# Kernel tuning notes

Hardware: AMD Instinct MI355X
Metric: run time of the kernel (lower is better)

## Reference

```python
import jax, jax.numpy as jnp
import numpy as np

EPS_BN = 1e-5

def conv1(W, x):
    # 1x1 conv1d, no bias: W (Cout,Cin), x (B,Cin,N)
    return jnp.einsum('oc,bcn->bon', W, x)

def bn(x, g, b):
    # training-mode BatchNorm1d over (batch, points) per channel
    m = jnp.mean(x, axis=(0, 2), keepdims=True)
    v = jnp.mean((x - m) ** 2, axis=(0, 2), keepdims=True)
    return g[None, :, None] * (x - m) / jnp.sqrt(v + EPS_BN) + b[None, :, None]

def three_interpolation(p_dense, p_sparse, f_sparse):
    # p_dense (B,N1,3), p_sparse (B,N2,3), f_sparse (B,C,N2) -> (B,C,N1)
    d2 = jnp.sum((p_dense[:, :, None, :] - p_sparse[:, None, :, :]) ** 2, axis=-1)  # (B,N1,N2)
    neg, idx = jax.lax.top_k(-d2, 3)  # 3 nearest neighbors, (B,N1,3)
    w = 1.0 / (jnp.maximum(-neg, 0.0) + 1e-8)  # inverse (squared) distance, as pointnet2 three_nn
    w = w / jnp.sum(w, axis=-1, keepdims=True)
    gathered = jax.vmap(lambda f, i: f[:, i])(f_sparse, idx)  # (B,C,N1,3)
    return jnp.einsum('bcnk,bnk->bcn', gathered, w)

def fp(p_dense, f_skip, p_sparse, f_sparse, W1, g1, b1, W2, g2, b2):
    # FeaturePropogation upsample branch: concat(skip, interp) -> [conv1d+BN] x decoder_layers (act_args=None)
    x = jnp.concatenate([f_skip, three_interpolation(p_dense, p_sparse, f_sparse)], axis=1)
    x = bn(conv1(W1, x), g1, b1)
    x = bn(conv1(W2, x), g2, b2)
    return x

def setup_inputs():
    key = jax.random.key(0)
    ks = iter(jax.random.split(key, 40))
    B, N = 4, 8192
    Ns = [N, N, 2048, 512, 128]      # point counts of p0..p4 (strides 4)
    Cs = [128, 256, 512, 1024]       # encoder_channel_list
    d = {}
    for i in range(5):
        d[f'p{i}'] = jax.random.normal(next(ks), (B, Ns[i], 3), jnp.float32)
    for i in range(4):
        d[f'f{i + 1}'] = jax.random.normal(next(ks), (B, Cs[i], Ns[i + 1]), jnp.float32)
    d['cls_label'] = jax.random.randint(next(ks), (B, 1), 0, 16)
    # class-label convs: 16 -> 64 (BN+GELU) -> C0
    d['Wc1'] = jax.random.normal(next(ks), (64, 16), jnp.float32) * 0.1
    d['gc'] = jax.random.uniform(next(ks), (64,), jnp.float32, 0.5, 1.5)
    d['bc'] = jax.random.normal(next(ks), (64,), jnp.float32) * 0.1
    d['Wc2'] = jax.random.normal(next(ks), (Cs[0], 64), jnp.float32) * 0.1
    # decoder stages, coarsest (s2) to finest (s0)
    ins = [Cs[2] + Cs[3], Cs[1] + Cs[2], Cs[0] + Cs[1]]
    outs = [Cs[2], Cs[1], Cs[0]]
    for tag, ci, co in zip(['s2', 's1', 's0'], ins, outs):
        d[f'W{tag}a'] = jax.random.normal(next(ks), (co, ci), jnp.float32) * 0.05
        d[f'g{tag}a'] = jax.random.uniform(next(ks), (co,), jnp.float32, 0.5, 1.5)
        d[f'b{tag}a'] = jax.random.normal(next(ks), (co,), jnp.float32) * 0.1
        d[f'W{tag}b'] = jax.random.normal(next(ks), (co, co), jnp.float32) * 0.05
        d[f'g{tag}b'] = jax.random.uniform(next(ks), (co,), jnp.float32, 0.5, 1.5)
        d[f'b{tag}b'] = jax.random.normal(next(ks), (co,), jnp.float32) * 0.1
    return d

def reference(p0, p1, p2, p3, p4, f1, f2, f3, f4, cls_label,
              Wc1, gc, bc, Wc2,
              Ws2a, gs2a, bs2a, Ws2b, gs2b, bs2b,
              Ws1a, gs1a, bs1a, Ws1b, gs1b, bs1b,
              Ws0a, gs0a, bs0a, Ws0b, gs0b, bs0b):
    B, N = p0.shape[0], p0.shape[1]
    # one-hot class embedding broadcast over points, mapped 16 -> 64 -> C0
    one_hot = jax.nn.one_hot(cls_label[:, 0], 16, dtype=f1.dtype)  # (B,16)
    cls_feat = jnp.broadcast_to(one_hot[:, :, None], (B, 16, N))
    cls_feat = conv1(Wc2, jax.nn.gelu(bn(conv1(Wc1, cls_feat), gc, bc), approximate=False))
    # decoder stages, coarse to fine
    f3n = fp(p3, f3, p4, f4, Ws2a, gs2a, bs2a, Ws2b, gs2b, bs2b)   # (B,512,512)
    f2n = fp(p2, f2, p3, f3n, Ws1a, gs1a, bs1a, Ws1b, gs1b, bs1b)  # (B,256,2048)
    f1n = fp(p1, f1 + cls_feat, p2, f2n, Ws0a, gs0a, bs0a, Ws0b, gs0b, bs0b)  # (B,128,8192)
    return f1n
```

## Files before the change

### kernel.cpp

```cpp
#include <hip/hip_runtime.h>
#include <math.h>

#define BN_EPS 1e-5f

typedef float f32x4 __attribute__((ext_vector_type(4)));
typedef short s16x8 __attribute__((ext_vector_type(8)));

__device__ __forceinline__ unsigned short f2bf(float f) {
    unsigned u = __builtin_bit_cast(unsigned, f);
    u = u + 0x7FFFu + ((u >> 16) & 1u);
    return (unsigned short)(u >> 16);
}
__device__ __forceinline__ float bf2f(unsigned short s) {
    unsigned u = ((unsigned)s) << 16;
    return __builtin_bit_cast(float, u);
}

__device__ __forceinline__ void gload16(const void* g, void* l) {
    __builtin_amdgcn_global_load_lds((const __attribute__((address_space(1))) unsigned int*)g,
                                     (__attribute__((address_space(3))) unsigned int*)l,
                                     16, 0, 0);
}

template<int CAND, int CHUNK, int STRIDE, bool PART>
__device__ __forceinline__ void knn_body(const float* __restrict__ pd,
                                         const float* __restrict__ ps,
                                         int N1, int N2total, int grp, int slice, int b,
                                         int* __restrict__ idx, float* __restrict__ w,
                                         unsigned long long* __restrict__ pk, int nslice,
                                         float* spx, float* spy, float* spz) {
    int tid = threadIdx.x;
    int cbase = slice * CAND;
    for (int g = tid; g < CAND; g += 256) {
        int s = g / CHUNK, off = g % CHUNK;
        size_t base = ((size_t)b * N2total + cbase + g) * 3;
        spx[s * STRIDE + off] = ps[base];
        spy[s * STRIDE + off] = ps[base + 1];
        spz[s * STRIDE + off] = ps[base + 2];
    }
    __syncthreads();
    int sub = tid & 7;
    int n = grp * 32 + (tid >> 3);
    size_t pb = ((size_t)b * N1 + n) * 3;
    float px = pd[pb], py = pd[pb + 1], pz = pd[pb + 2];
    float dd0 = 3.4e38f, dd1 = 3.4e38f, dd2 = 3.4e38f;
    int ii0 = 0, ii1 = 0, ii2 = 0;
    const float* rx = spx + sub * STRIDE;
    const float* ry = spy + sub * STRIDE;
    const float* rz = spz + sub * STRIDE;
    int jbase = cbase + sub * CHUNK;
    for (int t = 0; t < CHUNK; t += 4) {
        f32x4 x4 = *(const f32x4*)(rx + t);
        f32x4 y4 = *(const f32x4*)(ry + t);
        f32x4 z4 = *(const f32x4*)(rz + t);
#pragma unroll
        for (int e = 0; e < 4; e++) {
            float dx = px - x4[e], dy = py - y4[e], dz = pz - z4[e];
            float d = dx * dx + dy * dy + dz * dz;
            int j = jbase + t + e;
            bool C0 = d < dd0, C1 = d < dd1, C2 = d < dd2;
            int ni2 = C1 ? ii1 : (C2 ? j : ii2);
            int ni1 = C0 ? ii0 : (C1 ? j : ii1);
            int ni0 = C0 ? j : ii0;
            dd2 = __builtin_amdgcn_fmed3f(d, dd1, dd2);
            dd1 = __builtin_amdgcn_fmed3f(d, dd0, dd1);
            dd0 = fminf(d, dd0);
            ii0 = ni0; ii1 = ni1; ii2 = ni2;
        }
    }
    unsigned long long k0 = ((unsigned long long)__builtin_bit_cast(unsigned, dd0) << 32) | (unsigned)ii0;
    unsigned long long k1 = ((unsigned long long)__builtin_bit_cast(unsigned, dd1) << 32) | (unsigned)ii1;
    unsigned long long k2 = ((unsigned long long)__builtin_bit_cast(unsigned, dd2) << 32) | (unsigned)ii2;
#pragma unroll
    for (int m = 1; m < 8; m <<= 1) {
        unsigned long long e0, e1, e2;
        { int lo = __shfl_xor((int)(unsigned)(k0 & 0xFFFFFFFFull), m), hi = __shfl_xor((int)(unsigned)(k0 >> 32), m);
          e0 = ((unsigned long long)(unsigned)hi << 32) | (unsigned)lo; }
        { int lo = __shfl_xor((int)(unsigned)(k1 & 0xFFFFFFFFull), m), hi = __shfl_xor((int)(unsigned)(k1 >> 32), m);
          e1 = ((unsigned long long)(unsigned)hi << 32) | (unsigned)lo; }
        { int lo = __shfl_xor((int)(unsigned)(k2 & 0xFFFFFFFFull), m), hi = __shfl_xor((int)(unsigned)(k2 >> 32), m);
          e2 = ((unsigned long long)(unsigned)hi << 32) | (unsigned)lo; }
        unsigned long long t0, t1;
        t0 = k0 > e0 ? k0 : e0; k0 = k0 < e0 ? k0 : e0; t1 = k1 > t0 ? k1 : t0; k1 = k1 < t0 ? k1 : t0; k2 = k2 < t1 ? k2 : t1;
        t0 = k0 > e1 ? k0 : e1; k0 = k0 < e1 ? k0 : e1; t1 = k1 > t0 ? k1 : t0; k1 = k1 < t0 ? k1 : t0; k2 = k2 < t1 ? k2 : t1;
        t0 = k0 > e2 ? k0 : e2; k0 = k0 < e2 ? k0 : e2; t1 = k1 > t0 ? k1 : t0; k1 = k1 < t0 ? k1 : t0; k2 = k2 < t1 ? k2 : t1;
    }
    if (sub == 0) {
        if (PART) {
            size_t o = ((size_t)(b * N1 + n) * nslice + slice) * 3;
            pk[o] = k0; pk[o + 1] = k1; pk[o + 2] = k2;
        } else {
            float f0 = __builtin_bit_cast(float, (unsigned)(k0 >> 32));
            float f1 = __builtin_bit_cast(float, (unsigned)(k1 >> 32));
            float f2 = __builtin_bit_cast(float, (unsigned)(k2 >> 32));
            float w0 = 1.f / (f0 + 1e-8f), w1 = 1.f / (f1 + 1e-8f), w2 = 1.f / (f2 + 1e-8f);
            float s = 1.f / (w0 + w1 + w2);
            size_t o = ((size_t)b * N1 + n) * 3;
            idx[o] = (int)(unsigned)(k0 & 0xFFFFFFFFull);
            idx[o + 1] = (int)(unsigned)(k1 & 0xFFFFFFFFull);
            idx[o + 2] = (int)(unsigned)(k2 & 0xFFFFFFFFull);
            w[o] = w0 * s; w[o + 1] = w1 * s; w[o + 2] = w2 * s;
        }
    }
}

__global__ __launch_bounds__(256) void prep(const float* __restrict__ f1,
                                            const float* __restrict__ f2,
                                            const float* __restrict__ f3,
                                            const float* __restrict__ f4,
                                            unsigned short* __restrict__ F1T,
                                            unsigned short* __restrict__ F2T,
                                            unsigned short* __restrict__ F3T,
                                            unsigned short* __restrict__ F4T,
                                            const int* __restrict__ lbl,
                                            const float* __restrict__ Wc1,
                                            const float* __restrict__ gc,
                                            const float* __restrict__ bc,
                                            const float* __restrict__ Wc2,
                                            const float* __restrict__ p1,
                                            const float* __restrict__ p2,
                                            const float* __restrict__ p3,
                                            const float* __restrict__ p4,
                                            int* __restrict__ idx1, float* __restrict__ w1,
                                            int* __restrict__ idx2, float* __restrict__ w2,
                                            unsigned long long* __restrict__ pk0,
                                            const float* __restrict__ Ws2a,
                                            unsigned short* __restrict__ WI2, float* __restrict__ BIA2,
                                            unsigned short* __restrict__ WS2, float* __restrict__ BIS2,
                                            const float* __restrict__ Ws1a,
                                            unsigned short* __restrict__ WS1, float* __restrict__ BIS1,
                                            const float* __restrict__ Ws0a,
                                            unsigned short* __restrict__ WS0, float* __restrict__ BIS0) {
    __shared__ float t[32][33];
    __shared__ float clsv[32];
    __shared__ float hsh[4][64];
    __shared__ float actsh[4][64];
    __shared__ float spx[8 * 72], spy[8 * 72], spz[8 * 72];
    int bx = blockIdx.x, b = blockIdx.y;
    int tid = threadIdx.x;

    if (bx >= 3024) {
        if (b != 0) return;
        int wx = bx - 3024;
        const float* W; unsigned short* Wb; float* bias; int Ktot, kOff, Ks, m;
        if (wx < 512)       { W = Ws2a; Wb = WI2; bias = BIA2; Ktot = 1536; kOff = 512; Ks = 1024; m = wx; }
        else if (wx < 1024) { W = Ws2a; Wb = WS2; bias = BIS2; Ktot = 1536; kOff = 0;   Ks = 512;  m = wx - 512; }
        else if (wx < 1280) { W = Ws1a; Wb = WS1; bias = BIS1; Ktot = 768;  kOff = 0;   Ks = 256;  m = wx - 1024; }
        else                { W = Ws0a; Wb = WS0; bias = BIS0; Ktot = 384;  kOff = 0;   Ks = 128;  m = wx - 1280; }
        for (int k = tid; k < Ks; k += 256)
            Wb[(size_t)m * Ks + k] = f2bf(W[(size_t)m * Ktot + kOff + k]);
        if (tid == 0) bias[m] = 0.f;
        return;
    }
    if (bx >= 1920) {
        int kx = bx - 1920;
        if (kx < 16)      knn_body<128, 16, 24, false>(p3, p4, 512, 128, kx, 0, b, idx2, w2, nullptr, 1, spx, spy, spz);
        else if (kx < 80) knn_body<512, 64, 72, false>(p2, p3, 2048, 512, kx - 16, 0, b, idx1, w1, nullptr, 1, spx, spy, spz);
        else {
            int u = kx - 80;
            knn_body<512, 64, 72, true>(p1, p2, 8192, 2048, u >> 2, u & 3, b, nullptr, nullptr, pk0, 4, spx, spy, spz);
        }
        return;
    }
    const float* in; unsigned short* out; int C, N, nx, seg; bool docls = false;
    if (bx < 128)      { in = f4; out = F4T; C = 1024; N = 128;  nx = 4;   seg = bx; }
    else if (bx < 384) { in = f3; out = F3T; C = 512;  N = 512;  nx = 16;  seg = bx - 128; }
    else if (bx < 896) { in = f2; out = F2T; C = 256;  N = 2048; nx = 64;  seg = bx - 384; }
    else               { in = f1; out = F1T; C = 128;  N = 8192; nx = 256; seg = bx - 896; docls = true; }
    int n0 = (seg % nx) * 32, c0 = (seg / nx) * 32;
    if (docls) {
        { int b2 = tid >> 6, c = tid & 63; hsh[b2][c] = Wc1[c * 16 + lbl[b2]]; }
        __syncthreads();
        if (tid < 64) {
            int c = tid;
            float m = 0.f;
            for (int b2 = 0; b2 < 4; b2++) m += hsh[b2][c];
            m *= 0.25f;
            float v = 0.f;
            for (int b2 = 0; b2 < 4; b2++) { float d = hsh[b2][c] - m; v += d * d; }
            v *= 0.25f;
            float sc = gc[c] * rsqrtf(v + BN_EPS);
            float sh = bc[c] - m * sc;
            for (int b2 = 0; b2 < 4; b2++) {
                float x = hsh[b2][c] * sc + sh;
                actsh[b2][c] = 0.5f * x * (1.f + erff(x * 0.70710678118654752f));
            }
        }
        __syncthreads();
        if (tid < 32) {
            float s = 0.f;
            for (int c = 0; c < 64; c++) s += Wc2[(size_t)(c0 + tid) * 64 + c] * actsh[b][c];
            clsv[tid] = s;
        }
        __syncthreads();
    }
    int i = tid & 31, jj = tid >> 5;
#pragma unroll
    for (int j = jj; j < 32; j += 8) {
        float v = in[((size_t)b * C + c0 + j) * N + n0 + i];
        if (docls) v += clsv[j];
        t[j][i] = v;
    }
    __syncthreads();
    int j2 = tid & 31, i2b = tid >> 5;
#pragma unroll
    for (int i2 = i2b; i2 < 32; i2 += 8)
        out[((size_t)b * N + n0 + i2) * C + c0 + j2] = f2bf(t[j2][i2]);
}

__global__ __launch_bounds__(256) void knn_merge(const unsigned long long* __restrict__ pk,
                                                 int* __restrict__ idx, float* __restrict__ w,
                                                 int NQ) {
    int q = blockIdx.x * 256 + threadIdx.x;
    if (q >= NQ) return;
    const unsigned long long* p = pk + (size_t)q * 12;
    unsigned long long k0 = ~0ull, k1 = ~0ull, k2 = ~0ull;
#pragma unroll
    for (int i = 0; i < 12; i++) {
        unsigned long long c = p[i];
        unsigned long long t0 = k0 > c ? k0 : c; k0 = k0 < c ? k0 : c;
        unsigned long long t1 = k1 > t0 ? k1 : t0; k1 = k1 < t0 ? k1 : t0;
        k2 = k2 < t1 ? k2 : t1;
    }
    float f0 = __builtin_bit_cast(float, (unsigned)(k0 >> 32));
    float f1 = __builtin_bit_cast(float, (unsigned)(k1 >> 32));
    float f2 = __builtin_bit_cast(float, (unsigned)(k2 >> 32));
    float w0 = 1.f / (f0 + 1e-8f), w1 = 1.f / (f1 + 1e-8f), w2 = 1.f / (f2 + 1e-8f);
    float s = 1.f / (w0 + w1 + w2);
    size_t o = (size_t)q * 3;
    idx[o] = (int)(unsigned)(k0 & 0xFFFFFFFFull);
    idx[o + 1] = (int)(unsigned)(k1 & 0xFFFFFFFFull);
    idx[o + 2] = (int)(unsigned)(k2 & 0xFFFFFFFFull);
    w[o] = w0 * s; w[o + 1] = w1 * s; w[o + 2] = w2 * s;
}

__global__ __launch_bounds__(256) void wprep(const float* __restrict__ W,
                                             const float* __restrict__ sc,
                                             const float* __restrict__ sh,
                                             unsigned short* __restrict__ Wb,
                                             float* __restrict__ bias,
                                             int Ktot, int kOff, int Ks) {
    int m = blockIdx.x;
    int tid = threadIdx.x;
    float bsum = 0.f;
    for (int k = tid; k < Ks; k += 256) {
        float wv = W[(size_t)m * Ktot + kOff + k];
        Wb[(size_t)m * Ks + k] = f2bf(wv * sc[k]);
        bsum += wv * sh[k];
    }
    __shared__ float ls[256];
    ls[tid] = bsum;
    __syncthreads();
    for (int o = 128; o > 0; o >>= 1) {
        if (tid < o) ls[tid] += ls[tid + o];
        __syncthreads();
    }
    if (tid == 0) bias[m] = ls[0];
}

template<bool GATHER, bool WRSTATS>
__global__ __launch_bounds__(256) void gemm64(const unsigned short* __restrict__ XT,
                                              const unsigned short* __restrict__ Wb,
                                              const float* __restrict__ bias,
                                              const unsigned short* __restrict__ G,
                                              const int* __restrict__ gidx,
                                              const float* __restrict__ gw,
                                              int n1shift, int N2loc,
                                              unsigned short* __restrict__ OutT,
                                              float* __restrict__ ps,
                                              int BN, int K, int M) {
    __shared__ unsigned short As[2][64 * 32];
    __shared__ unsigned short Bs[2][64 * 32];
    __shared__ float sred[2][2][32][2];
    int tid = threadIdx.x;
    int lane = tid & 63, wid = tid >> 6;
    int wn = wid & 1, wm = wid >> 1;
    int bx = blockIdx.x, by = blockIdx.y;

    int srow = (wid << 4) + (lane >> 2);
    int skcol = (lane & 3) << 3;
    const unsigned short* gA = XT + (size_t)(bx * 64 + srow) * K + skcol;
    const unsigned short* gB = Wb + (size_t)(by * 64 + srow) * K + skcol;

    int r16 = lane & 15, q = lane >> 4;
    f32x4 acc[2][2];
#pragma unroll
    for (int i = 0; i < 2; i++)
#pragma unroll
        for (int j = 0; j < 2; j++) acc[i][j] = (f32x4)0.f;

    int nt = K >> 5;
    gload16(gA, &As[0][wid * 512]);
    gload16(gB, &Bs[0][wid * 512]);

    for (int t = 0; t < nt; t++) {
        int cur = t & 1;
        if (t + 1 < nt) {
            int k0 = (t + 1) << 5;
            gload16(gA + k0, &As[cur ^ 1][wid * 512]);
            gload16(gB + k0, &Bs[cur ^ 1][wid * 512]);
            asm volatile("s_waitcnt vmcnt(2)" ::: "memory");
        } else {
            asm volatile("s_waitcnt vmcnt(0)" ::: "memory");
        }
        __syncthreads();
        s16x8 afr[2], bfr[2];
        afr[0] = *(const s16x8*)&As[cur][(wn * 32 + r16) * 32 + q * 8];
        afr[1] = *(const s16x8*)&As[cur][(wn * 32 + 16 + r16) * 32 + q * 8];
        bfr[0] = *(const s16x8*)&Bs[cur][(wm * 32 + r16) * 32 + q * 8];
        bfr[1] = *(const s16x8*)&Bs[cur][(wm * 32 + 16 + r16) * 32 + q * 8];
        asm volatile("s_waitcnt lgkmcnt(0)" ::: "memory");
        __builtin_amdgcn_sched_barrier(0);
        __syncthreads();
#pragma unroll
        for (int i = 0; i < 2; i++)
#pragma unroll
            for (int j = 0; j < 2; j++)
                acc[i][j] = __builtin_amdgcn_mfma_f32_16x16x32_bf16(afr[i], bfr[j], acc[i][j], 0, 0, 0);
    }

    if (GATHER) {
#pragma unroll
        for (int i = 0; i < 2; i++)
#pragma unroll
            for (int rr = 0; rr < 4; rr++) {
                int R = bx * 64 + wn * 32 + i * 16 + q * 4 + rr;
                size_t ob = (size_t)R * 3;
                int i0 = gidx[ob], i1 = gidx[ob + 1], i2 = gidx[ob + 2];
                float w0 = gw[ob], w1 = gw[ob + 1], w2 = gw[ob + 2];
                size_t gbase = (size_t)(R >> n1shift) * N2loc;
                const unsigned short* g0 = G + (gbase + i0) * M + by * 64;
                const unsigned short* g1 = G + (gbase + i1) * M + by * 64;
                const unsigned short* g2 = G + (gbase + i2) * M + by * 64;
#pragma unroll
                for (int j = 0; j < 2; j++) {
                    int mcol = wm * 32 + j * 16 + r16;
                    acc[i][j][rr] += w0 * bf2f(g0[mcol]) + w1 * bf2f(g1[mcol]) + w2 * bf2f(g2[mcol]);
                }
            }
    }

    int mc0 = by * 64 + wm * 32 + r16;
    float bv[2] = { bias[mc0], bias[mc0 + 16] };
    unsigned short* Ob = OutT + (size_t)(bx * 64) * M + by * 64;
    float s[2] = {0.f, 0.f}, qq[2] = {0.f, 0.f};
#pragma unroll
    for (int i = 0; i < 2; i++) {
#pragma unroll
        for (int j = 0; j < 2; j++) {
            int mcol = wm * 32 + j * 16 + r16;
#pragma unroll
            for (int r = 0; r < 4; r++) {
                float v = acc[i][j][r] + bv[j];
                s[j] += v; qq[j] += v * v;
                int n = wn * 32 + i * 16 + q * 4 + r;
                Ob[(size_t)n * M + mcol] = f2bf(v);
            }
        }
    }
    if (WRSTATS) {
#pragma unroll
        for (int j = 0; j < 2; j++) {
            s[j] += __shfl_xor(s[j], 16); s[j] += __shfl_xor(s[j], 32);
            qq[j] += __shfl_xor(qq[j], 16); qq[j] += __shfl_xor(qq[j], 32);
        }
        if (lane < 16) {
#pragma unroll
            for (int j = 0; j < 2; j++) {
                sred[wn][wm][j * 16 + lane][0] = s[j];
                sred[wn][wm][j * 16 + lane][1] = qq[j];
            }
        }
        __syncthreads();
        if (tid < 64) {
            int wmm = tid >> 5, c = tid & 31;
            float ssum = sred[0][wmm][c][0] + sred[1][wmm][c][0];
            float qsum = sred[0][wmm][c][1] + sred[1][wmm][c][1];
            size_t blin = (size_t)by * gridDim.x + bx;
            ps[blin * 128 + tid * 2] = ssum;
            ps[blin * 128 + tid * 2 + 1] = qsum;
        }
    }
}

__global__ __launch_bounds__(256) void bn_finalize(const float* __restrict__ ps,
                                                   const float* __restrict__ g,
                                                   const float* __restrict__ bb,
                                                   float* __restrict__ sc,
                                                   float* __restrict__ sh,
                                                   int gx, int Npts) {
    int m = blockIdx.x;
    int by = m >> 6, ch = m & 63;
    float s = 0.f, q = 0.f;
    for (int bxi = threadIdx.x; bxi < gx; bxi += 256) {
        size_t blin = (size_t)by * gx + bxi;
        s += ps[blin * 128 + ch * 2];
        q += ps[blin * 128 + ch * 2 + 1];
    }
    __shared__ float ls[256], lq[256];
    ls[threadIdx.x] = s; lq[threadIdx.x] = q;
    __syncthreads();
    for (int o = 128; o > 0; o >>= 1) {
        if (threadIdx.x < o) { ls[threadIdx.x] += ls[threadIdx.x + o]; lq[threadIdx.x] += lq[threadIdx.x + o]; }
        __syncthreads();
    }
    if (threadIdx.x == 0) {
        float inv = 1.f / (float)Npts;
        float mean = ls[0] * inv;
        float var = fmaxf(lq[0] * inv - mean * mean, 0.f);
        float scale = g[m] * rsqrtf(var + BN_EPS);
        sc[m] = scale;
        sh[m] = bb[m] - mean * scale;
    }
}

__global__ __launch_bounds__(256) void out_bn_tr(const unsigned short* __restrict__ in,
                                                 float* __restrict__ out,
                                                 const float* __restrict__ sc,
                                                 const float* __restrict__ sh,
                                                 int M, int N) {
    __shared__ float t[32][33];
    int b = blockIdx.z;
    int n0 = blockIdx.x * 32, m0 = blockIdx.y * 32;
    int j = threadIdx.x & 31, ii = threadIdx.x >> 5;
#pragma unroll
    for (int i = ii; i < 32; i += 8)
        t[i][j] = bf2f(in[((size_t)b * N + n0 + i) * M + m0 + j]);
    __syncthreads();
    int i2 = threadIdx.x & 31, j2b = threadIdx.x >> 5;
#pragma unroll
    for (int j2 = j2b; j2 < 32; j2 += 8)
        out[((size_t)b * M + m0 + j2) * N + n0 + i2] = t[i2][j2] * sc[m0 + j2] + sh[m0 + j2];
}

extern "C" void kernel_launch(void* const* d_in, const int* in_sizes, int n_in,
                              void* d_out, int out_size, void* d_ws, size_t ws_size,
                              hipStream_t stream) {
    const float* p1 = (const float*)d_in[1];
    const float* p2 = (const float*)d_in[2];
    const float* p3 = (const float*)d_in[3];
    const float* p4 = (const float*)d_in[4];
    const float* f1 = (const float*)d_in[5];
    const float* f2 = (const float*)d_in[6];
    const float* f3 = (const float*)d_in[7];
    const float* f4 = (const float*)d_in[8];
    const int* cls = (const int*)d_in[9];
    const float* Wc1 = (const float*)d_in[10];
    const float* gc  = (const float*)d_in[11];
    const float* bc  = (const float*)d_in[12];
    const float* Wc2 = (const float*)d_in[13];
    const float* Ws2a = (const float*)d_in[14];
    const float* gs2a = (const float*)d_in[15];
    const float* bs2a = (const float*)d_in[16];
    const float* Ws2b = (const float*)d_in[17];
    const float* gs2b = (const float*)d_in[18];
    const float* bs2b = (const float*)d_in[19];
    const float* Ws1a = (const float*)d_in[20];
    const float* gs1a = (const float*)d_in[21];
    const float* bs1a = (const float*)d_in[22];
    const float* Ws1b = (const float*)d_in[23];
    const float* gs1b = (const float*)d_in[24];
    const float* bs1b = (const float*)d_in[25];
    const float* Ws0a = (const float*)d_in[26];
    const float* gs0a = (const float*)d_in[27];
    const float* bs0a = (const float*)d_in[28];
    const float* Ws0b = (const float*)d_in[29];
    const float* gs0b = (const float*)d_in[30];
    const float* bs0b = (const float*)d_in[31];

    char* ws = (char*)d_ws;
    size_t off = 0;
    auto alloc = [&](size_t bytes) { char* p = ws + off; off += (bytes + 255) & ~(size_t)255; return p; };
    unsigned short* F4T = (unsigned short*)alloc((size_t)4 * 128 * 1024 * 2);
    unsigned short* F3T = (unsigned short*)alloc((size_t)4 * 512 * 512 * 2);
    unsigned short* F2T = (unsigned short*)alloc((size_t)4 * 2048 * 256 * 2);
    unsigned short* F1T = (unsigned short*)alloc((size_t)4 * 8192 * 128 * 2);
    unsigned short* G2T = (unsigned short*)alloc((size_t)4 * 128 * 512 * 2);
    unsigned short* G1T = (unsigned short*)alloc((size_t)4 * 512 * 256 * 2);
    unsigned short* G0T = (unsigned short*)alloc((size_t)4 * 2048 * 128 * 2);
    unsigned short* YA  = (unsigned short*)alloc((size_t)4 * 8192 * 128 * 2);
    unsigned short* FN2 = (unsigned short*)alloc((size_t)4 * 512 * 512 * 2);
    unsigned short* FN1 = (unsigned short*)alloc((size_t)4 * 2048 * 256 * 2);
    unsigned short* XO  = (unsigned short*)alloc((size_t)4 * 8192 * 128 * 2);
    unsigned short* WI2 = (unsigned short*)alloc((size_t)512 * 1024 * 2);
    unsigned short* WS2 = (unsigned short*)alloc((size_t)512 * 512 * 2);
    unsigned short* WB2b = (unsigned short*)alloc((size_t)512 * 512 * 2);
    unsigned short* WI1 = (unsigned short*)alloc((size_t)256 * 512 * 2);
    unsigned short* WS1 = (unsigned short*)alloc((size_t)256 * 256 * 2);
    unsigned short* WB1b = (unsigned short*)alloc((size_t)256 * 256 * 2);
    unsigned short* WI0 = (unsigned short*)alloc((size_t)128 * 256 * 2);
    unsigned short* WS0 = (unsigned short*)alloc((size_t)128 * 128 * 2);
    unsigned short* WB0b = (unsigned short*)alloc((size_t)128 * 128 * 2);
    float* BIA2 = (float*)alloc(512 * 4); float* BIS2 = (float*)alloc(512 * 4);
    float* BI2b = (float*)alloc(512 * 4);
    float* BIA1 = (float*)alloc(256 * 4); float* BIS1 = (float*)alloc(256 * 4);
    float* BI1b = (float*)alloc(256 * 4);
    float* BIA0 = (float*)alloc(128 * 4); float* BIS0 = (float*)alloc(128 * 4);
    float* BI0b = (float*)alloc(128 * 4);
    int*   IDX0 = (int*)alloc((size_t)4 * 8192 * 3 * 4);
    float* WGT0 = (float*)alloc((size_t)4 * 8192 * 3 * 4);
    int*   IDX1 = (int*)alloc((size_t)4 * 2048 * 3 * 4);
    float* WGT1 = (float*)alloc((size_t)4 * 2048 * 3 * 4);
    int*   IDX2 = (int*)alloc((size_t)4 * 512 * 3 * 4);
    float* WGT2 = (float*)alloc((size_t)4 * 512 * 3 * 4);
    unsigned long long* PK0 = (unsigned long long*)alloc((size_t)4 * 8192 * 4 * 3 * 8);
    float* PS = (float*)alloc((size_t)1024 * 128 * 4);
    float* SC2a = (float*)alloc(512 * 4); float* SH2a = (float*)alloc(512 * 4);
    float* SC2b = (float*)alloc(512 * 4); float* SH2b = (float*)alloc(512 * 4);
    float* SC1a = (float*)alloc(512 * 4); float* SH1a = (float*)alloc(512 * 4);
    float* SC1b = (float*)alloc(512 * 4); float* SH1b = (float*)alloc(512 * 4);
    float* SC0a = (float*)alloc(512 * 4); float* SH0a = (float*)alloc(512 * 4);
    float* SC0b = (float*)alloc(512 * 4); float* SH0b = (float*)alloc(512 * 4);
    float* OUT = (float*)d_out;

    prep<<<dim3(4432, 4), 256, 0, stream>>>(f1, f2, f3, f4, F1T, F2T, F3T, F4T,
                                            cls, Wc1, gc, bc, Wc2,
                                            p1, p2, p3, p4,
                                            IDX1, WGT1, IDX2, WGT2, PK0,
                                            Ws2a, WI2, BIA2, WS2, BIS2,
                                            Ws1a, WS1, BIS1, Ws0a, WS0, BIS0);
    knn_merge<<<(4 * 8192) / 256, 256, 0, stream>>>(PK0, IDX0, WGT0, 4 * 8192);

    gemm64<false, false><<<dim3(8, 8), 256, 0, stream>>>(F4T, WI2, BIA2, nullptr, nullptr, nullptr, 0, 0,
                                                         G2T, nullptr, 512, 1024, 512);
    gemm64<true, true><<<dim3(32, 8), 256, 0, stream>>>(F3T, WS2, BIS2, G2T, IDX2, WGT2, 9, 128,
                                                        YA, PS, 2048, 512, 512);
    bn_finalize<<<512, 256, 0, stream>>>(PS, gs2a, bs2a, SC2a, SH2a, 32, 2048);
    wprep<<<512, 256, 0, stream>>>(Ws2b, SC2a, SH2a, WB2b, BI2b, 512, 0, 512);
    gemm64<false, true><<<dim3(32, 8), 256, 0, stream>>>(YA, WB2b, BI2b, nullptr, nullptr, nullptr, 0, 0,
                                                         FN2, PS, 2048, 512, 512);
    bn_finalize<<<512, 256, 0, stream>>>(PS, gs2b, bs2b, SC2b, SH2b, 32, 2048);

    wprep<<<256, 256, 0, stream>>>(Ws1a, SC2b, SH2b, WI1, BIA1, 768, 256, 512);
    gemm64<false, false><<<dim3(32, 4), 256, 0, stream>>>(FN2, WI1, BIA1, nullptr, nullptr, nullptr, 0, 0,
                                                          G1T, nullptr, 2048, 512, 256);
    gemm64<true, true><<<dim3(128, 4), 256, 0, stream>>>(F2T, WS1, BIS1, G1T, IDX1, WGT1, 11, 512,
                                                         YA, PS, 8192, 256, 256);
    bn_finalize<<<256, 256, 0, stream>>>(PS, gs1a, bs1a, SC1a, SH1a, 128, 8192);
    wprep<<<256, 256, 0, stream>>>(Ws1b, SC1a, SH1a, WB1b, BI1b, 256, 0, 256);
    gemm64<false, true><<<dim3(128, 4), 256, 0, stream>>>(YA, WB1b, BI1b, nullptr, nullptr, nullptr, 0, 0,
                                                          FN1, PS, 8192, 256, 256);
    bn_finalize<<<256, 256, 0, stream>>>(PS, gs1b, bs1b, SC1b, SH1b, 128, 8192);

    wprep<<<128, 256, 0, stream>>>(Ws0a, SC1b, SH1b, WI0, BIA0, 384, 128, 256);
    gemm64<false, false><<<dim3(128, 2), 256, 0, stream>>>(FN1, WI0, BIA0, nullptr, nullptr, nullptr, 0, 0,
                                                           G0T, nullptr, 8192, 256, 128);
    gemm64<true, true><<<dim3(512, 2), 256, 0, stream>>>(F1T, WS0, BIS0, G0T, IDX0, WGT0, 13, 2048,
                                                         YA, PS, 32768, 128, 128);
    bn_finalize<<<128, 256, 0, stream>>>(PS, gs0a, bs0a, SC0a, SH0a, 512, 32768);
    wprep<<<128, 256, 0, stream>>>(Ws0b, SC0a, SH0a, WB0b, BI0b, 128, 0, 128);
    gemm64<false, true><<<dim3(512, 2), 256, 0, stream>>>(YA, WB0b, BI0b, nullptr, nullptr, nullptr, 0, 0,
                                                          XO, PS, 32768, 128, 128);
    bn_finalize<<<128, 256, 0, stream>>>(PS, gs0b, bs0b, SC0b, SH0b, 512, 32768);

    out_bn_tr<<<dim3(8192 / 32, 128 / 32, 4), 256, 0, stream>>>(XO, OUT, SC0b, SH0b, 128, 8192);
}
```

Before: 186.8 us.

## Fuse BN finalize into weight prep and drop the separate kNN merge kernel

The finest-level kNN no longer splits candidates into four slices with a separate merge kernel. Each block now loops over all 2048 sparse points in LDS-staged slices, writing indices and weights directly. Separately, the bn_finalize kernels that fed the weight folding are merged into a new wprep_fin kernel, which reduces the partial sums itself before scaling the weights. This cuts about ten launches and an intermediate buffer, but every wprep_fin block recomputes the BN statistics redundantly, and the kNN now runs with four times fewer blocks, each doing four times the work.

```diff
diff --git a/kernel.cpp b/kernel.cpp
--- a/kernel.cpp
+++ b/kernel.cpp
@@ -22,50 +22,51 @@
                                      16, 0, 0);
 }
 
-template<int CAND, int CHUNK, int STRIDE, bool PART>
-__device__ __forceinline__ void knn_body(const float* __restrict__ pd,
+template<int N2TOT, int SLICE, int CHUNK, int STRIDE>
+__device__ __forceinline__ void knn_full(const float* __restrict__ pd,
                                          const float* __restrict__ ps,
-                                         int N1, int N2total, int grp, int slice, int b,
+                                         int N1, int grp, int b,
                                          int* __restrict__ idx, float* __restrict__ w,
-                                         unsigned long long* __restrict__ pk, int nslice,
                                          float* spx, float* spy, float* spz) {
     int tid = threadIdx.x;
-    int cbase = slice * CAND;
-    for (int g = tid; g < CAND; g += 256) {
-        int s = g / CHUNK, off = g % CHUNK;
-        size_t base = ((size_t)b * N2total + cbase + g) * 3;
-        spx[s * STRIDE + off] = ps[base];
-        spy[s * STRIDE + off] = ps[base + 1];
-        spz[s * STRIDE + off] = ps[base + 2];
-    }
-    __syncthreads();
     int sub = tid & 7;
     int n = grp * 32 + (tid >> 3);
     size_t pb = ((size_t)b * N1 + n) * 3;
     float px = pd[pb], py = pd[pb + 1], pz = pd[pb + 2];
     float dd0 = 3.4e38f, dd1 = 3.4e38f, dd2 = 3.4e38f;
     int ii0 = 0, ii1 = 0, ii2 = 0;
-    const float* rx = spx + sub * STRIDE;
-    const float* ry = spy + sub * STRIDE;
-    const float* rz = spz + sub * STRIDE;
-    int jbase = cbase + sub * CHUNK;
-    for (int t = 0; t < CHUNK; t += 4) {
-        f32x4 x4 = *(const f32x4*)(rx + t);
-        f32x4 y4 = *(const f32x4*)(ry + t);
-        f32x4 z4 = *(const f32x4*)(rz + t);
-#pragma unroll
-        for (int e = 0; e < 4; e++) {
-            float dx = px - x4[e], dy = py - y4[e], dz = pz - z4[e];
-            float d = dx * dx + dy * dy + dz * dz;
-            int j = jbase + t + e;
-            bool C0 = d < dd0, C1 = d < dd1, C2 = d < dd2;
-            int ni2 = C1 ? ii1 : (C2 ? j : ii2);
-            int ni1 = C0 ? ii0 : (C1 ? j : ii1);
-            int ni0 = C0 ? j : ii0;
-            dd2 = __builtin_amdgcn_fmed3f(d, dd1, dd2);
-            dd1 = __builtin_amdgcn_fmed3f(d, dd0, dd1);
-            dd0 = fminf(d, dd0);
-            ii0 = ni0; ii1 = ni1; ii2 = ni2;
+    for (int sb = 0; sb < N2TOT; sb += SLICE) {
+        __syncthreads();
+        for (int g = tid; g < SLICE; g += 256) {
+            int s = g / CHUNK, off = g % CHUNK;
+            size_t base = ((size_t)b * N2TOT + sb + g) * 3;
+            spx[s * STRIDE + off] = ps[base];
+            spy[s * STRIDE + off] = ps[base + 1];
+            spz[s * STRIDE + off] = ps[base + 2];
+        }
+        __syncthreads();
+        const float* rx = spx + sub * STRIDE;
+        const float* ry = spy + sub * STRIDE;
+        const float* rz = spz + sub * STRIDE;
+        int jbase = sb + sub * CHUNK;
+        for (int t = 0; t < CHUNK; t += 4) {
+            f32x4 x4 = *(const f32x4*)(rx + t);
+            f32x4 y4 = *(const f32x4*)(ry + t);
+            f32x4 z4 = *(const f32x4*)(rz + t);
+#pragma unroll
+            for (int e = 0; e < 4; e++) {
+                float dx = px - x4[e], dy = py - y4[e], dz = pz - z4[e];
+                float d = dx * dx + dy * dy + dz * dz;
+                int j = jbase + t + e;
+                bool C0 = d < dd0, C1 = d < dd1, C2 = d < dd2;
+                int ni2 = C1 ? ii1 : (C2 ? j : ii2);
+                int ni1 = C0 ? ii0 : (C1 ? j : ii1);
+                int ni0 = C0 ? j : ii0;
+                dd2 = __builtin_amdgcn_fmed3f(d, dd1, dd2);
+                dd1 = __builtin_amdgcn_fmed3f(d, dd0, dd1);
+                dd0 = fminf(d, dd0);
+                ii0 = ni0; ii1 = ni1; ii2 = ni2;
+            }
         }
     }
     unsigned long long k0 = ((unsigned long long)__builtin_bit_cast(unsigned, dd0) << 32) | (unsigned)ii0;
@@ -86,21 +87,16 @@
         t0 = k0 > e2 ? k0 : e2; k0 = k0 < e2 ? k0 : e2; t1 = k1 > t0 ? k1 : t0; k1 = k1 < t0 ? k1 : t0; k2 = k2 < t1 ? k2 : t1;
     }
     if (sub == 0) {
-        if (PART) {
-            size_t o = ((size_t)(b * N1 + n) * nslice + slice) * 3;
-            pk[o] = k0; pk[o + 1] = k1; pk[o + 2] = k2;
-        } else {
-            float f0 = __builtin_bit_cast(float, (unsigned)(k0 >> 32));
-            float f1 = __builtin_bit_cast(float, (unsigned)(k1 >> 32));
-            float f2 = __builtin_bit_cast(float, (unsigned)(k2 >> 32));
-            float w0 = 1.f / (f0 + 1e-8f), w1 = 1.f / (f1 + 1e-8f), w2 = 1.f / (f2 + 1e-8f);
-            float s = 1.f / (w0 + w1 + w2);
-            size_t o = ((size_t)b * N1 + n) * 3;
-            idx[o] = (int)(unsigned)(k0 & 0xFFFFFFFFull);
-            idx[o + 1] = (int)(unsigned)(k1 & 0xFFFFFFFFull);
-            idx[o + 2] = (int)(unsigned)(k2 & 0xFFFFFFFFull);
-            w[o] = w0 * s; w[o + 1] = w1 * s; w[o + 2] = w2 * s;
-        }
+        float f0 = __builtin_bit_cast(float, (unsigned)(k0 >> 32));
+        float f1 = __builtin_bit_cast(float, (unsigned)(k1 >> 32));
+        float f2 = __builtin_bit_cast(float, (unsigned)(k2 >> 32));
+        float w0 = 1.f / (f0 + 1e-8f), w1 = 1.f / (f1 + 1e-8f), w2 = 1.f / (f2 + 1e-8f);
+        float s = 1.f / (w0 + w1 + w2);
+        size_t o = ((size_t)b * N1 + n) * 3;
+        idx[o] = (int)(unsigned)(k0 & 0xFFFFFFFFull);
+        idx[o + 1] = (int)(unsigned)(k1 & 0xFFFFFFFFull);
+        idx[o + 2] = (int)(unsigned)(k2 & 0xFFFFFFFFull);
+        w[o] = w0 * s; w[o + 1] = w1 * s; w[o + 2] = w2 * s;
     }
 }
 
@@ -121,9 +117,9 @@
                                             const float* __restrict__ p2,
                                             const float* __restrict__ p3,
                                             const float* __restrict__ p4,
+                                            int* __restrict__ idx0, float* __restrict__ w0,
                                             int* __restrict__ idx1, float* __restrict__ w1,
                                             int* __restrict__ idx2, float* __restrict__ w2,
-                                            unsigned long long* __restrict__ pk0,
                                             const float* __restrict__ Ws2a,
                                             unsigned short* __restrict__ WI2, float* __restrict__ BIA2,
                                             unsigned short* __restrict__ WS2, float* __restrict__ BIS2,
@@ -139,9 +135,9 @@
     int bx = blockIdx.x, b = blockIdx.y;
     int tid = threadIdx.x;
 
-    if (bx >= 3024) {
+    if (bx >= 2256) {
         if (b != 0) return;
-        int wx = bx - 3024;
+        int wx = bx - 2256;
         const float* W; unsigned short* Wb; float* bias; int Ktot, kOff, Ks, m;
         if (wx < 512)       { W = Ws2a; Wb = WI2; bias = BIA2; Ktot = 1536; kOff = 512; Ks = 1024; m = wx; }
         else if (wx < 1024) { W = Ws2a; Wb = WS2; bias = BIS2; Ktot = 1536; kOff = 0;   Ks = 512;  m = wx - 512; }
@@ -154,12 +150,9 @@
     }
     if (bx >= 1920) {
         int kx = bx - 1920;
-        if (kx < 16)      knn_body<128, 16, 24, false>(p3, p4, 512, 128, kx, 0, b, idx2, w2, nullptr, 1, spx, spy, spz);
-        else if (kx < 80) knn_body<512, 64, 72, false>(p2, p3, 2048, 512, kx - 16, 0, b, idx1, w1, nullptr, 1, spx, spy, spz);
-        else {
-            int u = kx - 80;
-            knn_body<512, 64, 72, true>(p1, p2, 8192, 2048, u >> 2, u & 3, b, nullptr, nullptr, pk0, 4, spx, spy, spz);
-        }
+        if (kx < 16)      knn_full<128, 128, 16, 24>(p3, p4, 512, kx, b, idx2, w2, spx, spy, spz);
+        else if (kx < 80) knn_full<512, 512, 64, 72>(p2, p3, 2048, kx - 16, b, idx1, w1, spx, spy, spz);
+        else              knn_full<2048, 512, 64, 72>(p1, p2, 8192, kx - 80, b, idx0, w0, spx, spy, spz);
         return;
     }
     const float* in; unsigned short* out; int C, N, nx, seg; bool docls = false;
@@ -208,45 +201,41 @@
         out[((size_t)b * N + n0 + i2) * C + c0 + j2] = f2bf(t[j2][i2]);
 }
 
-__global__ __launch_bounds__(256) void knn_merge(const unsigned long long* __restrict__ pk,
-                                                 int* __restrict__ idx, float* __restrict__ w,
-                                                 int NQ) {
-    int q = blockIdx.x * 256 + threadIdx.x;
-    if (q >= NQ) return;
-    const unsigned long long* p = pk + (size_t)q * 12;
-    unsigned long long k0 = ~0ull, k1 = ~0ull, k2 = ~0ull;
-#pragma unroll
-    for (int i = 0; i < 12; i++) {
-        unsigned long long c = p[i];
-        unsigned long long t0 = k0 > c ? k0 : c; k0 = k0 < c ? k0 : c;
-        unsigned long long t1 = k1 > t0 ? k1 : t0; k1 = k1 < t0 ? k1 : t0;
-        k2 = k2 < t1 ? k2 : t1;
-    }
-    float f0 = __builtin_bit_cast(float, (unsigned)(k0 >> 32));
-    float f1 = __builtin_bit_cast(float, (unsigned)(k1 >> 32));
-    float f2 = __builtin_bit_cast(float, (unsigned)(k2 >> 32));
-    float w0 = 1.f / (f0 + 1e-8f), w1 = 1.f / (f1 + 1e-8f), w2 = 1.f / (f2 + 1e-8f);
-    float s = 1.f / (w0 + w1 + w2);
-    size_t o = (size_t)q * 3;
-    idx[o] = (int)(unsigned)(k0 & 0xFFFFFFFFull);
-    idx[o + 1] = (int)(unsigned)(k1 & 0xFFFFFFFFull);
-    idx[o + 2] = (int)(unsigned)(k2 & 0xFFFFFFFFull);
-    w[o] = w0 * s; w[o + 1] = w1 * s; w[o + 2] = w2 * s;
-}
-
-__global__ __launch_bounds__(256) void wprep(const float* __restrict__ W,
-                                             const float* __restrict__ sc,
-                                             const float* __restrict__ sh,
-                                             unsigned short* __restrict__ Wb,
-                                             float* __restrict__ bias,
-                                             int Ktot, int kOff, int Ks) {
-    int m = blockIdx.x;
-    int tid = threadIdx.x;
+__global__ __launch_bounds__(256) void wprep_fin(const float* __restrict__ W,
+                                                 const float* __restrict__ ps,
+                                                 const float* __restrict__ g,
+                                                 const float* __restrict__ bb,
+                                                 unsigned short* __restrict__ Wb,
+                                                 float* __restrict__ bias,
+                                                 int Ktot, int kOff, int Ks,
+                                                 int gx, int Npts) {
+    __shared__ float scl[1024], shl[1024];
+    int m = blockIdx.x, tid = threadIdx.x;
+    for (int k0 = 0; k0 < Ks; k0 += 256) {
+        int k = k0 + tid;
+        if (k < Ks) {
+            float s = 0.f, q = 0.f;
+            size_t rowbase = (size_t)(k >> 6) * gx;
+            int ch2 = (k & 63) * 2;
+            for (int bxi = 0; bxi < gx; bxi++) {
+                size_t blin = rowbase + bxi;
+                s += ps[blin * 128 + ch2];
+                q += ps[blin * 128 + ch2 + 1];
+            }
+            float inv = 1.f / (float)Npts;
+            float mean = s * inv;
+            float var = fmaxf(q * inv - mean * mean, 0.f);
+            float scale = g[k] * rsqrtf(var + BN_EPS);
+            scl[k] = scale;
+            shl[k] = bb[k] - mean * scale;
+        }
+    }
+    __syncthreads();
     float bsum = 0.f;
     for (int k = tid; k < Ks; k += 256) {
         float wv = W[(size_t)m * Ktot + kOff + k];
-        Wb[(size_t)m * Ks + k] = f2bf(wv * sc[k]);
-        bsum += wv * sh[k];
+        Wb[(size_t)m * Ks + k] = f2bf(wv * scl[k]);
+        bsum += wv * shl[k];
     }
     __shared__ float ls[256];
     ls[tid] = bsum;
@@ -503,52 +492,40 @@
     float* WGT1 = (float*)alloc((size_t)4 * 2048 * 3 * 4);
     int*   IDX2 = (int*)alloc((size_t)4 * 512 * 3 * 4);
     float* WGT2 = (float*)alloc((size_t)4 * 512 * 3 * 4);
-    unsigned long long* PK0 = (unsigned long long*)alloc((size_t)4 * 8192 * 4 * 3 * 8);
     float* PS = (float*)alloc((size_t)1024 * 128 * 4);
-    float* SC2a = (float*)alloc(512 * 4); float* SH2a = (float*)alloc(512 * 4);
-    float* SC2b = (float*)alloc(512 * 4); float* SH2b = (float*)alloc(512 * 4);
-    float* SC1a = (float*)alloc(512 * 4); float* SH1a = (float*)alloc(512 * 4);
-    float* SC1b = (float*)alloc(512 * 4); float* SH1b = (float*)alloc(512 * 4);
-    float* SC0a = (float*)alloc(512 * 4); float* SH0a = (float*)alloc(512 * 4);
     float* SC0b = (float*)alloc(512 * 4); float* SH0b = (float*)alloc(512 * 4);
     float* OUT = (float*)d_out;
 
-    prep<<<dim3(4432, 4), 256, 0, stream>>>(f1, f2, f3, f4, F1T, F2T, F3T, F4T,
+    prep<<<dim3(3664, 4), 256, 0, stream>>>(f1, f2, f3, f4, F1T, F2T, F3T, F4T,
                                             cls, Wc1, gc, bc, Wc2,
                                             p1, p2, p3, p4,
-                                            IDX1, WGT1, IDX2, WGT2, PK0,
+                                            IDX0, WGT0, IDX1, WGT1, IDX2, WGT2,
                                             Ws2a, WI2, BIA2, WS2, BIS2,
                                             Ws1a, WS1, BIS1, Ws0a, WS0, BIS0);
-    knn_merge<<<(4 * 8192) / 256, 256, 0, stream>>>(PK0, IDX0, WGT0, 4 * 8192);
 
     gemm64<false, false><<<dim3(8, 8), 256, 0, stream>>>(F4T, WI2, BIA2, nullptr, nullptr, nullptr, 0, 0,
                                                          G2T, nullptr, 512, 1024, 512);
     gemm64<true, true><<<dim3(32, 8), 256, 0, stream>>>(F3T, WS2, BIS2, G2T, IDX2, WGT2, 9, 128,
                                                         YA, PS, 2048, 512, 512);
-    bn_finalize<<<512, 256, 0, stream>>>(PS, gs2a, bs2a, SC2a, SH2a, 32, 2048);
-    wprep<<<512, 256, 0, stream>>>(Ws2b, SC2a, SH2a, WB2b, BI2b, 512, 0, 512);
+    wprep_fin<<<512, 256, 0, stream>>>(Ws2b, PS, gs2a, bs2a, WB2b, BI2b, 512, 0, 512, 32, 2048);
     gemm64<false, true><<<dim3(32, 8), 256, 0, stream>>>(YA, WB2b, BI2b, nullptr, nullptr, nullptr, 0, 0,
                                                          FN2, PS, 2048, 512, 512);
-    bn_finalize<<<512, 256, 0, stream>>>(PS, gs2b, bs2b, SC2b, SH2b, 32, 2048);
-
-    wprep<<<256, 256, 0, stream>>>(Ws1a, SC2b, SH2b, WI1, BIA1, 768, 256, 512);
+    wprep_fin<<<256, 256, 0, stream>>>(Ws1a, PS, gs2b, bs2b, WI1, BIA1, 768, 256, 512, 32, 2048);
+
     gemm64<false, false><<<dim3(32, 4), 256, 0, stream>>>(FN2, WI1, BIA1, nullptr, nullptr, nullptr, 0, 0,
                                                           G1T, nullptr, 2048, 512, 256);
     gemm64<true, true><<<dim3(128, 4), 256, 0, stream>>>(F2T, WS1, BIS1, G1T, IDX1, WGT1, 11, 512,
                                                          YA, PS, 8192, 256, 256);
-    bn_finalize<<<256, 256, 0, stream>>>(PS, gs1a, bs1a, SC1a, SH1a, 128, 8192);
-    wprep<<<256, 256, 0, stream>>>(Ws1b, SC1a, SH1a, WB1b, BI1b, 256, 0, 256);
+    wprep_fin<<<256, 256, 0, stream>>>(Ws1b, PS, gs1a, bs1a, WB1b, BI1b, 256, 0, 256, 128, 8192);
     gemm64<false, true><<<dim3(128, 4), 256, 0, stream>>>(YA, WB1b, BI1b, nullptr, nullptr, nullptr, 0, 0,
                                                           FN1, PS, 8192, 256, 256);
-    bn_finalize<<<256, 256, 0, stream>>>(PS, gs1b, bs1b, SC1b, SH1b, 128, 8192);
-
-    wprep<<<128, 256, 0, stream>>>(Ws0a, SC1b, SH1b, WI0, BIA0, 384, 128, 256);
+    wprep_fin<<<128, 256, 0, stream>>>(Ws0a, PS, gs1b, bs1b, WI0, BIA0, 384, 128, 256, 128, 8192);
+
     gemm64<false, false><<<dim3(128, 2), 256, 0, stream>>>(FN1, WI0, BIA0, nullptr, nullptr, nullptr, 0, 0,
                                                            G0T, nullptr, 8192, 256, 128);
     gemm64<true, true><<<dim3(512, 2), 256, 0, stream>>>(F1T, WS0, BIS0, G0T, IDX0, WGT0, 13, 2048,
                                                          YA, PS, 32768, 128, 128);
-    bn_finalize<<<128, 256, 0, stream>>>(PS, gs0a, bs0a, SC0a, SH0a, 512, 32768);
-    wprep<<<128, 256, 0, stream>>>(Ws0b, SC0a, SH0a, WB0b, BI0b, 128, 0, 128);
+    wprep_fin<<<128, 256, 0, stream>>>(Ws0b, PS, gs0a, bs0a, WB0b, BI0b, 128, 0, 128, 512, 32768);
     gemm64<false, true><<<dim3(512, 2), 256, 0, stream>>>(YA, WB0b, BI0b, nullptr, nullptr, nullptr, 0, 0,
                                                           XO, PS, 32768, 128, 128);
     bn_finalize<<<128, 256, 0, stream>>>(PS, gs0b, bs0b, SC0b, SH0b, 512, 32768);
```

Result: slower. 392.6 us (+110.2%).
